# Performance work log

Measured on AMD Instinct MI355X. Metric: run time of the kernel, lower is better.

The kernel has to match this reference:

```python
import jax, jax.numpy as jnp
import numpy as np

B_SZ = 2; L = 512; D_MODEL = 1024
D_STATE = 128; HEADDIM = 64; NGROUPS = 1
D_INNER = 2048; D_SSM = 2048
NHEADS = D_SSM // HEADDIM          # 32
HPG = NHEADS // NGROUPS            # heads per group
HALF = D_STATE // 2
D_IN_PROJ = D_INNER + D_SSM + 2 * NGROUPS * D_STATE + NHEADS + NHEADS + NHEADS * HALF  # 6464
EPS = 1e-5

def _rms(v, w):
    return v * jax.lax.rsqrt(jnp.mean(v * v, axis=-1, keepdims=True) + EPS) * w

def _rope(v, c, s):
    v1, v2 = v[..., :HALF], v[..., HALF:]
    return jnp.concatenate([v1 * c - v2 * s, v2 * c + v1 * s], axis=-1)

def setup_inputs() -> dict:
    key = jax.random.key(0)
    ks = jax.random.split(key, 3)
    rng = np.random.default_rng(0)
    # dt_bias init per module: inverse-softplus of dt ~ LogUniform(dt_min, dt_max)
    dt = np.exp(rng.random(NHEADS) * (np.log(0.1) - np.log(0.001)) + np.log(0.001))
    dt = np.maximum(dt, 1e-4)
    dt_bias = (dt + np.log(-np.expm1(-dt))).astype(np.float32)
    A_log = np.log(rng.uniform(1.0, 16.0, NHEADS)).astype(np.float32)
    return {
        'u': jax.random.normal(ks[0], (B_SZ, L, D_MODEL), jnp.float32),
        'W_in': jax.random.normal(ks[1], (D_MODEL, D_IN_PROJ), jnp.float32) / np.sqrt(D_MODEL),
        'W_out': jax.random.normal(ks[2], (D_INNER, D_MODEL), jnp.float32) / np.sqrt(D_INNER),
        'dt_bias': jnp.asarray(dt_bias),
        'A_log': jnp.asarray(A_log),
        'D': jnp.ones((NHEADS,), jnp.float32),
        'B_bias': jnp.ones((NGROUPS * D_STATE,), jnp.float32),
        'C_bias': jnp.ones((NGROUPS * D_STATE,), jnp.float32),
        'B_norm_w': jnp.ones((D_STATE,), jnp.float32),
        'C_norm_w': jnp.ones((D_STATE,), jnp.float32),
        'norm_w': jnp.ones((D_SSM,), jnp.float32),
    }

def reference(u, W_in, W_out, dt_bias, A_log, D, B_bias, C_bias, B_norm_w, C_norm_w, norm_w):
    b, l, _ = u.shape
    zxbcdt = u @ W_in  # (b, l, d_in_proj)
    s0 = D_INNER; s1 = s0 + D_SSM
    s2 = s1 + NGROUPS * D_STATE; s3 = s2 + NGROUPS * D_STATE
    s4 = s3 + NHEADS; s5 = s4 + NHEADS
    z = zxbcdt[..., :s0]
    x = zxbcdt[..., s0:s1]
    Bv = zxbcdt[..., s1:s2]
    Cv = zxbcdt[..., s2:s3]
    dt_raw = zxbcdt[..., s3:s4]
    lam_raw = zxbcdt[..., s4:s5]
    theta = zxbcdt[..., s5:]
    # BC bias + QK RMSNorm
    Bg = _rms((Bv + B_bias).reshape(b, l, NGROUPS, D_STATE), B_norm_w)
    Cg = _rms((Cv + C_bias).reshape(b, l, NGROUPS, D_STATE), C_norm_w)
    # data-dependent RoPE with cumulative angles, averaged over heads per group
    cum = jnp.cumsum(theta.reshape(b, l, NHEADS, HALF), axis=1)
    cos = jnp.cos(cum).reshape(b, l, NGROUPS, HPG, HALF).mean(3)
    sin = jnp.sin(cum).reshape(b, l, NGROUPS, HPG, HALF).mean(3)
    Bg = _rope(Bg, cos, sin)
    Cg = _rope(Cg, cos, sin)
    # discretization
    dt = jax.nn.softplus(dt_raw + dt_bias)          # (b, l, nheads)
    dA = jnp.exp(dt * (-jnp.exp(A_log)))            # (b, l, nheads)
    x = jax.nn.silu(x).reshape(b, l, NHEADS, HEADDIM)
    # trapezoidal blending of x and B with previous step
    lam = jax.nn.sigmoid(lam_raw)                   # (b, l, nheads)
    x_prev = jnp.pad(x[:, :-1], ((0, 0), (1, 0), (0, 0), (0, 0)))
    x_eff = lam[..., None] * x + (1.0 - lam[..., None]) * x_prev
    B_prev = jnp.pad(Bg[:, :-1], ((0, 0), (1, 0), (0, 0), (0, 0)))
    lam_g = lam.reshape(b, l, NGROUPS, HPG).mean(-1)[..., None]
    B_eff = lam_g * Bg + (1.0 - lam_g) * B_prev
    # selective scan over time
    xs = jnp.moveaxis(x_eff.reshape(b, l, NGROUPS, HPG, HEADDIM), 1, 0)
    dAs = jnp.moveaxis(dA.reshape(b, l, NGROUPS, HPG), 1, 0)
    dts = jnp.moveaxis(dt.reshape(b, l, NGROUPS, HPG), 1, 0)
    Bs = jnp.moveaxis(B_eff, 1, 0)
    Cs = jnp.moveaxis(Cg, 1, 0)
    def step(h, inp):
        dA_t, dt_t, x_t, B_t, C_t = inp
        # h: (b, g, hpg, headdim, d_state)
        h = dA_t[..., None, None] * h + (dt_t[..., None] * x_t)[..., None] * B_t[:, :, None, None, :]
        y_t = jnp.einsum('bgnpd,bgd->bgnp', h, C_t)
        return h, y_t
    h0 = jnp.zeros((b, NGROUPS, HPG, HEADDIM, D_STATE), u.dtype)
    _, ys = jax.lax.scan(step, h0, (dAs, dts, xs, Bs, Cs))
    y = jnp.moveaxis(ys, 0, 1).reshape(b, l, NHEADS, HEADDIM) + D[None, None, :, None] * x_eff
    # gated RMSNorm (norm after gate), then output projection
    y = y.reshape(b, l, D_SSM) * jax.nn.silu(z)
    y = y * jax.lax.rsqrt(jnp.mean(y * y, axis=-1, keepdims=True) + EPS) * norm_w
    return y @ W_out
```

## Files before the change

### kernel.cpp

```cpp
#include <hip/hip_runtime.h>
#include <hip/hip_bf16.h>
#include <cstdint>

#define TOK 1024
#define LSEQ 512
#define DMODEL 1024
#define DPROJ 6464
#define DPROJP 6528
#define DSSM 2048
#define NHEADS 32
#define HEADDIM 64
#define DSTATE 128
#define NCH 8
#define CL 64

typedef __attribute__((ext_vector_type(4))) float f32x4;
typedef _Float16 f16;
typedef __attribute__((ext_vector_type(8))) _Float16 f16x8;
typedef __attribute__((ext_vector_type(4))) _Float16 f16x4;
typedef __attribute__((ext_vector_type(8))) ushort u16x8;

__device__ __forceinline__ float silu_f(float x){
  return x*__builtin_amdgcn_rcpf(1.f+__expf(-x));
}

__device__ __forceinline__ void gload16(const void* g, void* l){
  __builtin_amdgcn_global_load_lds(
      (const __attribute__((address_space(1))) unsigned int*)g,
      (__attribute__((address_space(3))) unsigned int*)l, 16, 0, 0);
}

__global__ __launch_bounds__(256) void prep_kernel(
    const float* __restrict__ W_in, const float* __restrict__ W_out,
    const float* __restrict__ u,
    f16* __restrict__ WT, f16* __restrict__ WoT, f16* __restrict__ uhf)
{
  int b = blockIdx.x;
  if (b < 6528 + 2048){
    __shared__ float tile[32][33];
    const float* W; f16* T; int K, N, bx, by;
    if (b < 6528){ W = W_in;  T = WT;  K = DMODEL; N = DPROJ;  bx = b % 204;      by = b / 204; }
    else         { int ib = b - 6528; W = W_out; T = WoT; K = DSSM; N = DMODEL; bx = ib & 31; by = ib >> 5; }
    int tx = threadIdx.x & 31, ty = threadIdx.x >> 5;
    int n = bx*32 + tx;
    #pragma unroll
    for (int i=0;i<4;i++){
      int k = by*32 + ty + i*8;
      tile[ty+i*8][tx] = (n < N) ? W[(size_t)k*N + n] : 0.f;
    }
    __syncthreads();
    #pragma unroll
    for (int i=0;i<4;i++){
      int nn = bx*32 + ty + i*8;
      int kk = by*32 + tx;
      T[(size_t)nn*K + kk] = (f16)tile[tx][ty+i*8];
    }
  } else {
    int i = (b - 8576)*256 + threadIdx.x;
    f32x4 v = ((const f32x4*)u)[i];
    f16x4 h;
    #pragma unroll
    for (int j=0;j<4;j++) h[j] = (f16)v[j];
    *(f16x4*)&uhf[(size_t)i*4] = h;
  }
}

__global__ __launch_bounds__(512) void gemmh_kernel(
    const f16* __restrict__ A, const f16* __restrict__ B,
    float* __restrict__ C, int K, int kLen, int ldc, int nbn, int chunk)
{
  __shared__ ushort sA[2][8192], sB[2][8192];
  int bid = blockIdx.x;
  int newL = (bid & 7)*chunk + (bid >> 3);
  int bm = newL & 7;
  int pan = newL >> 3;
  int bn = pan % nbn;
  int z  = pan / nbn;
  int k0 = z * kLen;
  C += (size_t)z * 1024 * ldc;

  int tid = threadIdx.x;
  int wid = tid >> 6, lane = tid & 63;
  int wr = wid >> 2, wc = wid & 3;
  int fr = lane & 15, kq = lane >> 4;
  f32x4 acc[4][2] = {};

  int srow = tid & 127;
  int skg  = (tid >> 7) & 3;
  const f16* gA = A + (size_t)(bm*128+srow)*K + k0 + skg*8;
  const f16* gB = B + (size_t)(bn*128+srow)*K + k0 + skg*8;

  int rA = kq*1024 + (wr*64 + fr)*8;
  int rB = kq*1024 + (wc*32 + fr)*8;
  int NK = kLen >> 6;

#define STAGE(buf, kk) { \
    const f16* pa = gA + (kk)*64; \
    const f16* pb = gB + (kk)*64; \
    gload16(pa,      &sA[buf][tid*8]); \
    gload16(pa + 32, &sA[buf][tid*8 + 4096]); \
    gload16(pb,      &sB[buf][tid*8]); \
    gload16(pb + 32, &sB[buf][tid*8 + 4096]); \
  }

  STAGE(0, 0)
  STAGE(1, 1)

  for (int ks=0; ks<NK; ks++){
    int cur = ks & 1;
    if (ks == NK-1) asm volatile("s_waitcnt vmcnt(0)" ::: "memory");
    else            asm volatile("s_waitcnt vmcnt(4)" ::: "memory");
    __builtin_amdgcn_s_barrier();
    f16x8 af0[4], af1[4], bf0[2], bf1[2];
    #pragma unroll
    for (int i=0;i<4;i++){
      af0[i] = *(const f16x8*)&sA[cur][rA + i*128];
      af1[i] = *(const f16x8*)&sA[cur][rA + 4096 + i*128];
    }
    #pragma unroll
    for (int j=0;j<2;j++){
      bf0[j] = *(const f16x8*)&sB[cur][rB + j*128];
      bf1[j] = *(const f16x8*)&sB[cur][rB + 4096 + j*128];
    }
    asm volatile("s_waitcnt lgkmcnt(0)" ::: "memory");
    __builtin_amdgcn_sched_barrier(0);
    __builtin_amdgcn_s_barrier();
    if (ks+2 < NK) STAGE(cur, ks+2)
    #pragma unroll
    for (int i=0;i<4;i++)
      #pragma unroll
      for (int j=0;j<2;j++)
        acc[i][j] = __builtin_amdgcn_mfma_f32_16x16x32_f16(af0[i], bf0[j], acc[i][j], 0,0,0);
    #pragma unroll
    for (int i=0;i<4;i++)
      #pragma unroll
      for (int j=0;j<2;j++)
        acc[i][j] = __builtin_amdgcn_mfma_f32_16x16x32_f16(af1[i], bf1[j], acc[i][j], 0,0,0);
  }
#undef STAGE
  int rq = kq * 4;
  #pragma unroll
  for (int i=0;i<4;i++){
    #pragma unroll
    for (int j=0;j<2;j++){
      int row = bm*128 + wr*64 + i*16 + rq;
      int col = bn*128 + wc*32 + j*16 + fr;
      #pragma unroll
      for (int q=0;q<4;q++)
        C[(size_t)(row+q)*ldc + col] = acc[i][j][q];
    }
  }
}

__global__ __launch_bounds__(256) void red4_kernel(const float* __restrict__ P, float* __restrict__ O){
  int i = blockIdx.x*256 + threadIdx.x;
  f32x4 v = ((const f32x4*)P)[i];
  v += ((const f32x4*)P)[i + 262144];
  v += ((const f32x4*)P)[i + 2*262144];
  v += ((const f32x4*)P)[i + 3*262144];
  ((f32x4*)O)[i] = v;
}

__global__ __launch_bounds__(256) void thT_kernel(const float* __restrict__ zx,
    float* __restrict__ thT)
{
  __shared__ float tile[64][65];
  int ci = blockIdx.x, li = blockIdx.y, bb = blockIdx.z;
  int tx = threadIdx.x & 63, ty = threadIdx.x >> 6;
  const float* src = zx + (size_t)(bb*LSEQ + li*64)*DPROJP + 4416 + ci*64;
  #pragma unroll
  for (int i=0;i<16;i++){
    int r = ty + i*4;
    tile[r][tx] = src[(size_t)r*DPROJP + tx];
  }
  __syncthreads();
  float* dst = thT + ((size_t)bb*2048 + ci*64)*512 + (size_t)li*64;
  #pragma unroll
  for (int i=0;i<16;i++){
    int r = ty + i*4;
    dst[(size_t)r*512 + tx] = tile[tx][r];
  }
}

__global__ __launch_bounds__(512) void cum2_kernel(const float* __restrict__ thT,
    float* __restrict__ cosm, float* __restrict__ sinm)
{
  __shared__ float wsum[8];
  int blk = blockIdx.x;
  int half = blk & 1, hd = (blk >> 1) & 63, b = blk >> 7;
  int l = threadIdx.x, lane = l & 63, w = l >> 6;
  float accc = 0.f, accs = 0.f;
  const float* base = thT + (size_t)b*2048*512 + (size_t)(half*16)*64*512 + (size_t)hd*512;
  for (int h = 0; h < 16; h++){
    float x = base[(size_t)h*64*512 + l];
    #pragma unroll
    for (int m=1; m<64; m<<=1){
      float v = __shfl_up(x, m, 64);
      if (lane >= m) x += v;
    }
    if (lane == 63) wsum[w] = x;
    __syncthreads();
    float pre = 0.f;
    for (int i=0;i<w;i++) pre += wsum[i];
    x += pre;
    float s, c;
    __sincosf(x, &s, &c);
    accc += c; accs += s;
    __syncthreads();
  }
  int t = b*LSEQ + l;
  cosm[half*TOK*64 + t*64+hd] = accc*(1.f/32.f);
  sinm[half*TOK*64 + t*64+hd] = accs*(1.f/32.f);
}

__global__ __launch_bounds__(256) void ew_kernel(const float* __restrict__ zx,
    const float* __restrict__ cosm, const float* __restrict__ sinm,
    const float* __restrict__ dt_bias, const float* __restrict__ A_log,
    const float* __restrict__ B_bias, const float* __restrict__ C_bias,
    const float* __restrict__ Bnw, const float* __restrict__ Cnw,
    f16* __restrict__ Bg, f16* __restrict__ Cg, float4* __restrict__ scal)
{
  int t = blockIdx.x; int tid = threadIdx.x;
  __shared__ float red[256];
  __shared__ float nb[128], nc[128];
  const float* row = zx + (size_t)t*DPROJP;
  float v;
  if (tid < 128) v = row[4096 + tid] + B_bias[tid];
  else           v = row[4224 + (tid-128)] + C_bias[tid-128];
  red[tid] = v*v;
  __syncthreads();
  #pragma unroll
  for (int s=64; s>0; s>>=1){
    if ((tid & 127) < s) red[tid] += red[tid + s];
    __syncthreads();
  }
  float ms = red[(tid < 128) ? 0 : 128] * (1.f/128.f);
  float rs = rsqrtf(ms + 1e-5f);
  float w  = (tid < 128) ? Bnw[tid] : Cnw[tid-128];
  float nv = v * rs * w;
  if (tid < 128) nb[tid] = nv; else nc[tid-128] = nv;
  __syncthreads();
  if (tid < 64){
    float c = cosm[t*64+tid] + cosm[TOK*64 + t*64+tid];
    float s = sinm[t*64+tid] + sinm[TOK*64 + t*64+tid];
    float a = nb[tid], bq = nb[tid+64];
    Bg[(size_t)t*128 + tid]      = (f16)(a*c - bq*s);
    Bg[(size_t)t*128 + 64 + tid] = (f16)(bq*c + a*s);
  } else if (tid < 128){
    int i = tid - 64;
    float c = cosm[t*64+i] + cosm[TOK*64 + t*64+i];
    float s = sinm[t*64+i] + sinm[TOK*64 + t*64+i];
    float a = nc[i], bq = nc[i+64];
    Cg[(size_t)t*128 + i]      = (f16)(a*c - bq*s);
    Cg[(size_t)t*128 + 64 + i] = (f16)(bq*c + a*s);
  } else if (tid < 160){
    int hh = tid - 128;
    float dtr = row[4352 + hh] + dt_bias[hh];
    float dtv = (dtr > 20.f) ? dtr : log1pf(expf(dtr));
    float dA  = expf(-dtv * expf(A_log[hh]));
    float lr  = row[4384 + hh];
    float lam = 1.f/(1.f + expf(-lr));
    float lg = lam;
    #pragma unroll
    for (int m=1;m<32;m<<=1) lg += __shfl_xor(lg, m, 64);
    lg *= (1.f/32.f);
    scal[(size_t)t*32 + hh] = make_float4(dtv, dA, lam, lg);
  }
}

#define CST 136
#define SST 72
__global__ __launch_bounds__(256, 2) void scanA_kernel(
    const float* __restrict__ zx, const f16* __restrict__ Bg,
    const f16* __restrict__ Cg, const float4* __restrict__ scal,
    const float* __restrict__ A_log, const float* __restrict__ Dp,
    float* __restrict__ ypart, float* __restrict__ hcarry,
    float* __restrict__ clog, float* __restrict__ AtotB)
{
  __shared__ __align__(16) f16 smC[64*CST];
  __shared__ __align__(16) f16 smB[64*CST];
  __shared__ __align__(16) f16 smBT[128*SST];
  __shared__ __align__(16) f16 smX[64*SST];
  __shared__ __align__(16) float sDt[64], sLam[64], sLg[64], sCl[64], sW[64];
  f16* sSp = smC;

  int blk = blockIdx.x;
  int c = blk & 7, h = (blk>>3)&31, b = blk>>8;
  int idx = blk;
  int t0 = b*LSEQ + c*CL;
  int tid = threadIdx.x;
  int w = tid >> 6, lane = tid & 63;
  int fr = lane & 15, kq = lane >> 4;

  {
    int s = tid >> 2, dq4 = (tid & 3) * 32;
    const ushort* src = (const ushort*)(Cg + (size_t)(t0+s)*128 + dq4);
    ushort* dst = (ushort*)(smC + s*CST + dq4);
    #pragma unroll
    for (int i=0;i<4;i++) *(u16x8*)(dst + i*8) = *(const u16x8*)(src + i*8);
  }
  if (tid < 64){
    float4 sc = scal[(size_t)(t0+tid)*32 + h];
    float a  = __expf(A_log[h]);
    float cl = -sc.x * a * 1.44269504088896f;
    #pragma unroll
    for (int m=1; m<64; m<<=1){
      float v = __shfl_up(cl, m, 64);
      if (lane >= m) cl += v;
    }
    float cl63 = __shfl(cl, 63, 64);
    sDt[tid] = sc.x; sLam[tid] = sc.z; sLg[tid] = sc.w;
    sCl[tid] = cl;
    sW[tid]  = exp2f(cl63 - cl) * sc.x;
    clog[(size_t)idx*64 + tid] = cl;
    if (tid == 63) AtotB[idx] = exp2f(cl63);
  }
  __syncthreads();

  {
    int s = tid >> 2, dq4 = (tid & 3) * 32;
    float lg = sLg[s], wgt = sW[s];
    bool zp = (s == 0 && c == 0);
    const f16* bc_p = Bg + (size_t)(t0+s)*128 + dq4;
    const f16* bp_p = Bg + (size_t)(t0+s-1)*128 + dq4;
    #pragma unroll
    for (int i=0;i<32;i+=4){
      f16x4 bc4 = *(const f16x4*)(bc_p + i);
      f16x4 bp4 = {0,0,0,0};
      if (!zp) bp4 = *(const f16x4*)(bp_p + i);
      f16x4 be4;
      #pragma unroll
      for (int e=0;e<4;e++){
        float bc = (float)bc4[e], bp = (float)bp4[e];
        float be = bp + lg*(bc - bp);
        be4[e] = (f16)be;
        smBT[(dq4+i+e)*SST + s] = (f16)(be * wgt);
      }
      *(f16x4*)(smB + s*CST + dq4 + i) = be4;
    }
  }
  {
    int p = tid & 63, sg = tid >> 6;
    int s0 = sg*16;
    const float* xbase = zx + 2048 + h*64 + p;
    float xp_ = 0.f;
    if (!(s0 == 0 && c == 0))
      xp_ = silu_f(xbase[(size_t)(t0+s0-1)*DPROJP]);
    #pragma unroll
    for (int i=0;i<16;i++){
      int s = s0 + i;
      float xs = silu_f(xbase[(size_t)(t0+s)*DPROJP]);
      smX[p*SST + s] = (f16)(xp_ + sLam[s]*(xs - xp_));
      xp_ = xs;
    }
  }
  __syncthreads();

  int tq = w >> 1, sq = w & 1;
  f32x4 acc1[2][2] = {};
  #pragma unroll
  for (int kt=0; kt<4; kt++){
    f16x8 ah[2], bh[2];
    #pragma unroll
    for (int i=0;i<2;i++)
      ah[i] = *(const f16x8*)&smC[(tq*32 + i*16 + fr)*CST + kt*32 + kq*8];
    #pragma unroll
    for (int j=0;j<2;j++)
      bh[j] = *(const f16x8*)&smB[(sq*32 + j*16 + fr)*CST + kt*32 + kq*8];
    #pragma unroll
    for (int i=0;i<2;i++)
      #pragma unroll
      for (int j=0;j<2;j++)
        acc1[i][j] = __builtin_amdgcn_mfma_f32_16x16x32_f16(ah[i], bh[j], acc1[i][j], 0,0,0);
  }
  #pragma unroll
  for (int i=0;i<2;i++){
    int tb = tq*32 + i*16 + kq*4;
    f32x4 clt = *(const f32x4*)&sCl[tb];
    #pragma unroll
    for (int j=0;j<2;j++){
      int scol = sq*32 + j*16 + fr;
      float cls = sCl[scol], dts = sDt[scol];
      #pragma unroll
      for (int q=0;q<4;q++){
        float m = (tb+q >= scol) ? exp2f(clt[q]-cls)*dts : 0.f;
        acc1[i][j][q] *= m;
      }
    }
  }
  __syncthreads();
  #pragma unroll
  for (int i=0;i<2;i++){
    int tb = tq*32 + i*16 + kq*4;
    #pragma unroll
    for (int j=0;j<2;j++){
      int scol = sq*32 + j*16 + fr;
      #pragma unroll
      for (int q=0;q<4;q++)
        sSp[(tb+q)*SST + scol] = (f16)acc1[i][j][q];
    }
  }
  __syncthreads();

  float Dh = Dp[h];
  {
    f32x4 acc2[2][2] = {};
    #pragma unroll
    for (int kt=0; kt<2; kt++){
      f16x8 ah[2], bh[2];
      #pragma unroll
      for (int i=0;i<2;i++)
        ah[i] = *(const f16x8*)&sSp[(tq*32 + i*16 + fr)*SST + kt*32 + kq*8];
      #pragma unroll
      for (int j=0;j<2;j++)
        bh[j] = *(const f16x8*)&smX[(sq*32 + j*16 + fr)*SST + kt*32 + kq*8];
      #pragma unroll
      for (int i=0;i<2;i++)
        #pragma unroll
        for (int j=0;j<2;j++)
          acc2[i][j] = __builtin_amdgcn_mfma_f32_16x16x32_f16(ah[i], bh[j], acc2[i][j], 0,0,0);
    }
    #pragma unroll
    for (int i=0;i<2;i++){
      int tb = tq*32 + i*16 + kq*4;
      #pragma unroll
      for (int j=0;j<2;j++){
        int pc = sq*32 + j*16 + fr;
        #pragma unroll
        for (int q=0;q<4;q++){
          float y = acc2[i][j][q] + Dh * (float)smX[pc*SST + tb + q];
          ypart[(size_t)(t0+tb+q)*DSSM + h*64 + pc] = y;
        }
      }
    }
  }

  {
    f32x4 acc4[2][4] = {};
    int ph = w >> 1, dh = w & 1;
    #pragma unroll
    for (int kt=0; kt<2; kt++){
      f16x8 ah[2], bh[4];
      #pragma unroll
      for (int i=0;i<2;i++)
        ah[i] = *(const f16x8*)&smX[(ph*32 + i*16 + fr)*SST + kt*32 + kq*8];
      #pragma unroll
      for (int j=0;j<4;j++)
        bh[j] = *(const f16x8*)&smBT[(dh*64 + j*16 + fr)*SST + kt*32 + kq*8];
      #pragma unroll
      for (int i=0;i<2;i++)
        #pragma unroll
        for (int j=0;j<4;j++)
          acc4[i][j] = __builtin_amdgcn_mfma_f32_16x16x32_f16(ah[i], bh[j], acc4[i][j], 0,0,0);
    }
    size_t hb = (size_t)idx * 64 * 128;
    #pragma unroll
    for (int i=0;i<2;i++){
      int pb = ph*32 + i*16 + kq*4;
      #pragma unroll
      for (int j=0;j<4;j++){
        int dc = dh*64 + j*16 + fr;
        #pragma unroll
        for (int q=0;q<4;q++)
          hcarry[hb + (size_t)(pb+q)*128 + dc] = acc4[i][j][q];
      }
    }
  }
}

__global__ __launch_bounds__(256) void scan2_kernel(float* __restrict__ hcarry,
    const float* __restrict__ AtotB)
{
  int idx = blockIdx.x*256 + threadIdx.x;
  int d = idx & 127, pp = (idx >> 7) & 63, h = (idx >> 13) & 31, b = idx >> 18;
  size_t base = ((size_t)(b*32+h)*512 + pp)*128 + d;
  float Hin = 0.f;
  #pragma unroll
  for (int c=0; c<NCH; c++){
    float Atot = AtotB[(b*32+h)*8 + c];
    float S = hcarry[base + (size_t)c*8192];
    hcarry[base + (size_t)c*8192] = Hin;
    Hin = Atot*Hin + S;
  }
}

__global__ __launch_bounds__(256) void scanB_kernel(
    const f16* __restrict__ Cg, const float* __restrict__ hcarry,
    const float* __restrict__ clog, float* __restrict__ ypart)
{
  __shared__ __align__(16) f16 smC[64*CST];
  __shared__ __align__(16) f16 smH[64*CST];
  __shared__ __align__(16) float sK[64];
  int blk = blockIdx.x;
  int c = blk & 7, h = (blk>>3)&31, b = blk>>8;
  int idx = blk;
  int t0 = b*LSEQ + c*CL;
  int tid = threadIdx.x;
  int w = tid >> 6, lane = tid & 63;
  int fr = lane & 15, kq = lane >> 4;
  {
    int s = tid >> 2, dq4 = (tid & 3) * 32;
    const ushort* src = (const ushort*)(Cg + (size_t)(t0+s)*128 + dq4);
    ushort* dst = (ushort*)(smC + s*CST + dq4);
    #pragma unroll
    for (int i=0;i<4;i++) *(u16x8*)(dst + i*8) = *(const u16x8*)(src + i*8);
    const float* hs = hcarry + (size_t)idx*8192 + (size_t)s*128 + dq4;
    #pragma unroll
    for (int i=0;i<32;i+=4){
      f32x4 v = *(const f32x4*)(hs + i);
      f16x4 hv;
      #pragma unroll
      for (int e=0;e<4;e++) hv[e] = (f16)v[e];
      *(f16x4*)(smH + s*CST + dq4 + i) = hv;
    }
  }
  if (tid < 64) sK[tid] = exp2f(clog[(size_t)idx*64 + tid]);
  __syncthreads();

  int tq = w >> 1, pq = w & 1;
  f32x4 acc[2][2] = {};
  #pragma unroll
  for (int kt=0; kt<4; kt++){
    f16x8 ah[2], bh[2];
    #pragma unroll
    for (int i=0;i<2;i++)
      ah[i] = *(const f16x8*)&smC[(tq*32 + i*16 + fr)*CST + kt*32 + kq*8];
    #pragma unroll
    for (int j=0;j<2;j++)
      bh[j] = *(const f16x8*)&smH[(pq*32 + j*16 + fr)*CST + kt*32 + kq*8];
    #pragma unroll
    for (int i=0;i<2;i++)
      #pragma unroll
      for (int j=0;j<2;j++)
        acc[i][j] = __builtin_amdgcn_mfma_f32_16x16x32_f16(ah[i], bh[j], acc[i][j], 0,0,0);
  }
  #pragma unroll
  for (int i=0;i<2;i++){
    int tb = tq*32 + i*16 + kq*4;
    f32x4 kv = *(const f32x4*)&sK[tb];
    #pragma unroll
    for (int j=0;j<2;j++){
      int pc = pq*32 + j*16 + fr;
      #pragma unroll
      for (int q=0;q<4;q++)
        ypart[(size_t)TOK*DSSM + (size_t)(t0+tb+q)*DSSM + h*64 + pc] = acc[i][j][q]*kv[q];
    }
  }
}

__global__ __launch_bounds__(256) void fin_kernel(const float* __restrict__ zx,
    const float* __restrict__ ypart, const float* __restrict__ normw,
    f16* __restrict__ yf)
{
  int t = blockIdx.x; int tid = threadIdx.x;
  __shared__ float red[256];
  float vloc[8];
  float ss = 0.f;
  #pragma unroll
  for (int i=0;i<8;i++){
    int cc = tid + i*256;
    float y = ypart[(size_t)t*DSSM + cc]
            + ypart[(size_t)(TOK + t)*DSSM + cc];
    float z = zx[(size_t)t*DPROJP + cc];
    float v = y * (z / (1.f + expf(-z)));
    vloc[i] = v; ss += v*v;
  }
  red[tid] = ss; __syncthreads();
  #pragma unroll
  for (int s=128; s>0; s>>=1){ if (tid < s) red[tid] += red[tid+s]; __syncthreads(); }
  float rs = rsqrtf(red[0]*(1.f/2048.f) + 1e-5f);
  #pragma unroll
  for (int i=0;i<8;i++){
    int cc = tid + i*256;
    yf[(size_t)t*DSSM + cc] = (f16)(vloc[i]*rs*normw[cc]);
  }
}

extern "C" void kernel_launch(void* const* d_in, const int* in_sizes, int n_in,
                              void* d_out, int out_size, void* d_ws, size_t ws_size,
                              hipStream_t stream)
{
  const float* u      = (const float*)d_in[0];
  const float* W_in   = (const float*)d_in[1];
  const float* W_out  = (const float*)d_in[2];
  const float* dt_bias= (const float*)d_in[3];
  const float* A_log  = (const float*)d_in[4];
  const float* Dp     = (const float*)d_in[5];
  const float* B_bias = (const float*)d_in[6];
  const float* C_bias = (const float*)d_in[7];
  const float* Bnw    = (const float*)d_in[8];
  const float* Cnw    = (const float*)d_in[9];
  const float* normw  = (const float*)d_in[10];
  float* out = (float*)d_out;

  char* ws = (char*)d_ws;
  size_t o = 0;
  auto alloc = [&](size_t bytes)->char*{
    char* r = ws + o; o = (o + bytes + 255) & ~(size_t)255; return r;
  };
  f16*  WT   = (f16*)alloc((size_t)DPROJP*DMODEL*2);
  f16*  WoT  = (f16*)alloc((size_t)DMODEL*DSSM*2);
  f16*  uhf  = (f16*)alloc((size_t)TOK*DMODEL*2);
  f16*  yf   = (f16*)alloc((size_t)TOK*DSSM*2);
  float*  zx   = (float*)alloc((size_t)TOK*DPROJP*4);
  float*  thT  = (float*)alloc((size_t)2*2048*512*4);
  float*  cosm = (float*)alloc((size_t)2*TOK*64*4);
  float*  sinm = (float*)alloc((size_t)2*TOK*64*4);
  f16*   Bgb  = (f16*)alloc((size_t)TOK*128*2);
  f16*   Cgb  = (f16*)alloc((size_t)TOK*128*2);
  float4* scal = (float4*)alloc((size_t)TOK*32*16);
  float*  ypart= (float*)alloc((size_t)2*TOK*DSSM*4);
  float*  hcarry=(float*)alloc((size_t)2*32*NCH*64*128*4);
  float*  clog = (float*)alloc((size_t)512*64*4);
  float*  AtotB= (float*)alloc((size_t)512*4);
  float*  Cpart =(float*)alloc((size_t)4*TOK*DMODEL*4);

  prep_kernel<<<dim3(9600), dim3(256), 0, stream>>>(W_in, W_out, u, WT, WoT, uhf);

  gemmh_kernel<<<dim3(408), dim3(512), 0, stream>>>(uhf, WT, zx, DMODEL, DMODEL, DPROJP, 51, 51);

  thT_kernel<<<dim3(32, 8, 2), dim3(256), 0, stream>>>(zx, thT);
  cum2_kernel<<<dim3(256), dim3(512), 0, stream>>>(thT, cosm, sinm);

  ew_kernel<<<dim3(TOK), dim3(256), 0, stream>>>(zx, cosm, sinm, dt_bias, A_log,
                                                 B_bias, C_bias, Bnw, Cnw, Bgb, Cgb, scal);

  scanA_kernel<<<dim3(512),  dim3(256), 0, stream>>>(zx, Bgb, Cgb, scal, A_log, Dp,
                                                     ypart, hcarry, clog, AtotB);
  scan2_kernel<<<dim3(2048), dim3(256), 0, stream>>>(hcarry, AtotB);
  scanB_kernel<<<dim3(512),  dim3(256), 0, stream>>>(Cgb, hcarry, clog, ypart);

  fin_kernel<<<dim3(TOK), dim3(256), 0, stream>>>(zx, ypart, normw, yf);

  gemmh_kernel<<<dim3(256), dim3(512), 0, stream>>>(yf, WoT, Cpart, DSSM, 512, DMODEL, 8, 32);
  red4_kernel<<<dim3(TOK*DMODEL/1024), dim3(256), 0, stream>>>(Cpart, out);
}
```

Baseline: 129.3 us.

## Store intermediates in fp16 and split cumulative theta pass into quarters

Converts several fp32 intermediate buffers (theta transpose, scan partial outputs, chunk carry states, split-K GEMM partials) to fp16 to halve their memory traffic. The cum2 kernel is split into four head-quarters with twice the blocks for more parallelism, and ew sums four partials. This trades accuracy: the theta values stored in fp16 before a cumulative sum over 512 steps, and the fp16 carry states, may lose precision.

```diff
diff --git a/kernel.cpp b/kernel.cpp
--- a/kernel.cpp
+++ b/kernel.cpp
@@ -65,9 +65,10 @@
   }
 }
 
+template<bool HOUT>
 __global__ __launch_bounds__(512) void gemmh_kernel(
     const f16* __restrict__ A, const f16* __restrict__ B,
-    float* __restrict__ C, int K, int kLen, int ldc, int nbn, int chunk)
+    void* __restrict__ Cv, int K, int kLen, int ldc, int nbn, int chunk)
 {
   __shared__ ushort sA[2][8192], sB[2][8192];
   int bid = blockIdx.x;
@@ -77,7 +78,7 @@
   int bn = pan % nbn;
   int z  = pan / nbn;
   int k0 = z * kLen;
-  C += (size_t)z * 1024 * ldc;
+  size_t zoff = (size_t)z * 1024 * ldc;
 
   int tid = threadIdx.x;
   int wid = tid >> 6, lane = tid & 63;
@@ -146,23 +147,30 @@
       int row = bm*128 + wr*64 + i*16 + rq;
       int col = bn*128 + wc*32 + j*16 + fr;
       #pragma unroll
-      for (int q=0;q<4;q++)
-        C[(size_t)(row+q)*ldc + col] = acc[i][j][q];
-    }
-  }
-}
-
-__global__ __launch_bounds__(256) void red4_kernel(const float* __restrict__ P, float* __restrict__ O){
+      for (int q=0;q<4;q++){
+        if constexpr (HOUT)
+          ((f16*)Cv)[zoff + (size_t)(row+q)*ldc + col] = (f16)acc[i][j][q];
+        else
+          ((float*)Cv)[zoff + (size_t)(row+q)*ldc + col] = acc[i][j][q];
+      }
+    }
+  }
+}
+
+__global__ __launch_bounds__(256) void red4_kernel(const f16* __restrict__ P, float* __restrict__ O){
   int i = blockIdx.x*256 + threadIdx.x;
-  f32x4 v = ((const f32x4*)P)[i];
-  v += ((const f32x4*)P)[i + 262144];
-  v += ((const f32x4*)P)[i + 2*262144];
-  v += ((const f32x4*)P)[i + 3*262144];
+  f16x4 a = ((const f16x4*)P)[i];
+  f16x4 b = ((const f16x4*)P)[i + 262144];
+  f16x4 c = ((const f16x4*)P)[i + 2*262144];
+  f16x4 d = ((const f16x4*)P)[i + 3*262144];
+  f32x4 v;
+  #pragma unroll
+  for (int j=0;j<4;j++) v[j] = (float)a[j] + (float)b[j] + (float)c[j] + (float)d[j];
   ((f32x4*)O)[i] = v;
 }
 
 __global__ __launch_bounds__(256) void thT_kernel(const float* __restrict__ zx,
-    float* __restrict__ thT)
+    f16* __restrict__ thT)
 {
   __shared__ float tile[64][65];
   int ci = blockIdx.x, li = blockIdx.y, bb = blockIdx.z;
@@ -174,25 +182,25 @@
     tile[r][tx] = src[(size_t)r*DPROJP + tx];
   }
   __syncthreads();
-  float* dst = thT + ((size_t)bb*2048 + ci*64)*512 + (size_t)li*64;
+  f16* dst = thT + ((size_t)bb*2048 + ci*64)*512 + (size_t)li*64;
   #pragma unroll
   for (int i=0;i<16;i++){
     int r = ty + i*4;
-    dst[(size_t)r*512 + tx] = tile[tx][r];
-  }
-}
-
-__global__ __launch_bounds__(512) void cum2_kernel(const float* __restrict__ thT,
+    dst[(size_t)r*512 + tx] = (f16)tile[tx][r];
+  }
+}
+
+__global__ __launch_bounds__(512) void cum2_kernel(const f16* __restrict__ thT,
     float* __restrict__ cosm, float* __restrict__ sinm)
 {
   __shared__ float wsum[8];
   int blk = blockIdx.x;
-  int half = blk & 1, hd = (blk >> 1) & 63, b = blk >> 7;
+  int q = blk & 3, hd = (blk >> 2) & 63, b = blk >> 8;
   int l = threadIdx.x, lane = l & 63, w = l >> 6;
   float accc = 0.f, accs = 0.f;
-  const float* base = thT + (size_t)b*2048*512 + (size_t)(half*16)*64*512 + (size_t)hd*512;
-  for (int h = 0; h < 16; h++){
-    float x = base[(size_t)h*64*512 + l];
+  const f16* base = thT + (size_t)b*2048*512 + (size_t)(q*8)*64*512 + (size_t)hd*512;
+  for (int h = 0; h < 8; h++){
+    float x = (float)base[(size_t)h*64*512 + l];
     #pragma unroll
     for (int m=1; m<64; m<<=1){
       float v = __shfl_up(x, m, 64);
@@ -209,8 +217,8 @@
     __syncthreads();
   }
   int t = b*LSEQ + l;
-  cosm[half*TOK*64 + t*64+hd] = accc*(1.f/32.f);
-  sinm[half*TOK*64 + t*64+hd] = accs*(1.f/32.f);
+  cosm[q*TOK*64 + t*64+hd] = accc*(1.f/32.f);
+  sinm[q*TOK*64 + t*64+hd] = accs*(1.f/32.f);
 }
 
 __global__ __launch_bounds__(256) void ew_kernel(const float* __restrict__ zx,
@@ -241,15 +249,15 @@
   if (tid < 128) nb[tid] = nv; else nc[tid-128] = nv;
   __syncthreads();
   if (tid < 64){
-    float c = cosm[t*64+tid] + cosm[TOK*64 + t*64+tid];
-    float s = sinm[t*64+tid] + sinm[TOK*64 + t*64+tid];
+    float c = cosm[t*64+tid] + cosm[TOK*64 + t*64+tid] + cosm[2*TOK*64 + t*64+tid] + cosm[3*TOK*64 + t*64+tid];
+    float s = sinm[t*64+tid] + sinm[TOK*64 + t*64+tid] + sinm[2*TOK*64 + t*64+tid] + sinm[3*TOK*64 + t*64+tid];
     float a = nb[tid], bq = nb[tid+64];
     Bg[(size_t)t*128 + tid]      = (f16)(a*c - bq*s);
     Bg[(size_t)t*128 + 64 + tid] = (f16)(bq*c + a*s);
   } else if (tid < 128){
     int i = tid - 64;
-    float c = cosm[t*64+i] + cosm[TOK*64 + t*64+i];
-    float s = sinm[t*64+i] + sinm[TOK*64 + t*64+i];
+    float c = cosm[t*64+i] + cosm[TOK*64 + t*64+i] + cosm[2*TOK*64 + t*64+i] + cosm[3*TOK*64 + t*64+i];
+    float s = sinm[t*64+i] + sinm[TOK*64 + t*64+i] + sinm[2*TOK*64 + t*64+i] + sinm[3*TOK*64 + t*64+i];
     float a = nc[i], bq = nc[i+64];
     Cg[(size_t)t*128 + i]      = (f16)(a*c - bq*s);
     Cg[(size_t)t*128 + 64 + i] = (f16)(bq*c + a*s);
@@ -274,7 +282,7 @@
     const float* __restrict__ zx, const f16* __restrict__ Bg,
     const f16* __restrict__ Cg, const float4* __restrict__ scal,
     const float* __restrict__ A_log, const float* __restrict__ Dp,
-    float* __restrict__ ypart, float* __restrict__ hcarry,
+    f16* __restrict__ ypart, f16* __restrict__ hcarry,
     float* __restrict__ clog, float* __restrict__ AtotB)
 {
   __shared__ __align__(16) f16 smC[64*CST];
@@ -429,7 +437,7 @@
         #pragma unroll
         for (int q=0;q<4;q++){
           float y = acc2[i][j][q] + Dh * (float)smX[pc*SST + tb + q];
-          ypart[(size_t)(t0+tb+q)*DSSM + h*64 + pc] = y;
+          ypart[(size_t)(t0+tb+q)*DSSM + h*64 + pc] = (f16)y;
         }
       }
     }
@@ -462,13 +470,13 @@
         int dc = dh*64 + j*16 + fr;
         #pragma unroll
         for (int q=0;q<4;q++)
-          hcarry[hb + (size_t)(pb+q)*128 + dc] = acc4[i][j][q];
+          hcarry[hb + (size_t)(pb+q)*128 + dc] = (f16)acc4[i][j][q];
       }
     }
   }
 }
 
-__global__ __launch_bounds__(256) void scan2_kernel(float* __restrict__ hcarry,
+__global__ __launch_bounds__(256) void scan2_kernel(f16* __restrict__ hcarry,
     const float* __restrict__ AtotB)
 {
   int idx = blockIdx.x*256 + threadIdx.x;
@@ -478,15 +486,15 @@
   #pragma unroll
   for (int c=0; c<NCH; c++){
     float Atot = AtotB[(b*32+h)*8 + c];
-    float S = hcarry[base + (size_t)c*8192];
-    hcarry[base + (size_t)c*8192] = Hin;
+    float S = (float)hcarry[base + (size_t)c*8192];
+    hcarry[base + (size_t)c*8192] = (f16)Hin;
     Hin = Atot*Hin + S;
   }
 }
 
 __global__ __launch_bounds__(256) void scanB_kernel(
-    const f16* __restrict__ Cg, const float* __restrict__ hcarry,
-    const float* __restrict__ clog, float* __restrict__ ypart)
+    const f16* __restrict__ Cg, const f16* __restrict__ hcarry,
+    const float* __restrict__ clog, f16* __restrict__ ypart)
 {
   __shared__ __align__(16) f16 smC[64*CST];
   __shared__ __align__(16) f16 smH[64*CST];
@@ -504,15 +512,10 @@
     ushort* dst = (ushort*)(smC + s*CST + dq4);
     #pragma unroll
     for (int i=0;i<4;i++) *(u16x8*)(dst + i*8) = *(const u16x8*)(src + i*8);
-    const float* hs = hcarry + (size_t)idx*8192 + (size_t)s*128 + dq4;
-    #pragma unroll
-    for (int i=0;i<32;i+=4){
-      f32x4 v = *(const f32x4*)(hs + i);
-      f16x4 hv;
-      #pragma unroll
-      for (int e=0;e<4;e++) hv[e] = (f16)v[e];
-      *(f16x4*)(smH + s*CST + dq4 + i) = hv;
-    }
+    const ushort* hs = (const ushort*)(hcarry + (size_t)idx*8192 + (size_t)s*128 + dq4);
+    ushort* hd = (ushort*)(smH + s*CST + dq4);
+    #pragma unroll
+    for (int i=0;i<4;i++) *(u16x8*)(hd + i*8) = *(const u16x8*)(hs + i*8);
   }
   if (tid < 64) sK[tid] = exp2f(clog[(size_t)idx*64 + tid]);
   __syncthreads();
@@ -543,13 +546,13 @@
       int pc = pq*32 + j*16 + fr;
       #pragma unroll
       for (int q=0;q<4;q++)
-        ypart[(size_t)TOK*DSSM + (size_t)(t0+tb+q)*DSSM + h*64 + pc] = acc[i][j][q]*kv[q];
+        ypart[(size_t)TOK*DSSM + (size_t)(t0+tb+q)*DSSM + h*64 + pc] = (f16)(acc[i][j][q]*kv[q]);
     }
   }
 }
 
 __global__ __launch_bounds__(256) void fin_kernel(const float* __restrict__ zx,
-    const float* __restrict__ ypart, const float* __restrict__ normw,
+    const f16* __restrict__ ypart, const float* __restrict__ normw,
     f16* __restrict__ yf)
 {
   int t = blockIdx.x; int tid = threadIdx.x;
@@ -559,8 +562,8 @@
   #pragma unroll
   for (int i=0;i<8;i++){
     int cc = tid + i*256;
-    float y = ypart[(size_t)t*DSSM + cc]
-            + ypart[(size_t)(TOK + t)*DSSM + cc];
+    float y = (float)ypart[(size_t)t*DSSM + cc]
+            + (float)ypart[(size_t)(TOK + t)*DSSM + cc];
     float z = zx[(size_t)t*DPROJP + cc];
     float v = y * (z / (1.f + expf(-z)));
     vloc[i] = v; ss += v*v;
@@ -603,24 +606,24 @@
   f16*  uhf  = (f16*)alloc((size_t)TOK*DMODEL*2);
   f16*  yf   = (f16*)alloc((size_t)TOK*DSSM*2);
   float*  zx   = (float*)alloc((size_t)TOK*DPROJP*4);
-  float*  thT  = (float*)alloc((size_t)2*2048*512*4);
-  float*  cosm = (float*)alloc((size_t)2*TOK*64*4);
-  float*  sinm = (float*)alloc((size_t)2*TOK*64*4);
+  f16*   thT  = (f16*)alloc((size_t)2*2048*512*2);
+  float*  cosm = (float*)alloc((size_t)4*TOK*64*4);
+  float*  sinm = (float*)alloc((size_t)4*TOK*64*4);
   f16*   Bgb  = (f16*)alloc((size_t)TOK*128*2);
   f16*   Cgb  = (f16*)alloc((size_t)TOK*128*2);
   float4* scal = (float4*)alloc((size_t)TOK*32*16);
-  float*  ypart= (float*)alloc((size_t)2*TOK*DSSM*4);
-  float*  hcarry=(float*)alloc((size_t)2*32*NCH*64*128*4);
+  f16*   ypart= (f16*)alloc((size_t)2*TOK*DSSM*2);
+  f16*   hcarry=(f16*)alloc((size_t)2*32*NCH*64*128*2);
   float*  clog = (float*)alloc((size_t)512*64*4);
   float*  AtotB= (float*)alloc((size_t)512*4);
-  float*  Cpart =(float*)alloc((size_t)4*TOK*DMODEL*4);
+  f16*   Cpart =(f16*)alloc((size_t)4*TOK*DMODEL*2);
 
   prep_kernel<<<dim3(9600), dim3(256), 0, stream>>>(W_in, W_out, u, WT, WoT, uhf);
 
-  gemmh_kernel<<<dim3(408), dim3(512), 0, stream>>>(uhf, WT, zx, DMODEL, DMODEL, DPROJP, 51, 51);
+  gemmh_kernel<false><<<dim3(408), dim3(512), 0, stream>>>(uhf, WT, zx, DMODEL, DMODEL, DPROJP, 51, 51);
 
   thT_kernel<<<dim3(32, 8, 2), dim3(256), 0, stream>>>(zx, thT);
-  cum2_kernel<<<dim3(256), dim3(512), 0, stream>>>(thT, cosm, sinm);
+  cum2_kernel<<<dim3(512), dim3(512), 0, stream>>>(thT, cosm, sinm);
 
   ew_kernel<<<dim3(TOK), dim3(256), 0, stream>>>(zx, cosm, sinm, dt_bias, A_log,
                                                  B_bias, C_bias, Bnw, Cnw, Bgb, Cgb, scal);
@@ -632,6 +635,6 @@
 
   fin_kernel<<<dim3(TOK), dim3(256), 0, stream>>>(zx, ypart, normw, yf);
 
-  gemmh_kernel<<<dim3(256), dim3(512), 0, stream>>>(yf, WoT, Cpart, DSSM, 512, DMODEL, 8, 32);
+  gemmh_kernel<true><<<dim3(256), dim3(512), 0, stream>>>(yf, WoT, Cpart, DSSM, 512, DMODEL, 8, 32);
   red4_kernel<<<dim3(TOK*DMODEL/1024), dim3(256), 0, stream>>>(Cpart, out);
 }
```

Measured after the change: 115.4 us. -10.7%, faster.
